# Kernel optimization log

Measured on AMD Instinct MI355X. Metric: run time of the kernel, lower is better.

The kernel has to match this reference:

```python
import jax, jax.numpy as jnp
import numpy as np

B, L, D_MODEL, N_HEADS = 2, 2048, 2048, 16
HEAD_DIM = D_MODEL // N_HEADS
EPS = 1e-6
ROPE_THETA = 10000.0


def rms_norm(x, scale):
    # normalize over head_dim, learnable per-dim scale (QKNorm)
    var = jnp.mean(jnp.square(x), axis=-1, keepdims=True)
    return x * jax.lax.rsqrt(var + EPS) * scale


def rope(x, offset=0):
    # x: [B, H, T, D]; rotate-half rotary embedding over flattened positions
    T, D = x.shape[-2], x.shape[-1]
    half = D // 2
    inv_freq = 1.0 / (ROPE_THETA ** (jnp.arange(0, half, dtype=jnp.float32) / half))
    pos = jnp.arange(T, dtype=jnp.float32) + offset
    ang = pos[:, None] * inv_freq[None, :]            # [T, half]
    cos, sin = jnp.cos(ang), jnp.sin(ang)
    x1, x2 = x[..., :half], x[..., half:]
    return jnp.concatenate([x1 * cos - x2 * sin, x1 * sin + x2 * cos], axis=-1)


def setup_inputs() -> dict:
    key = jax.random.key(0)
    ks = jax.random.split(key, 7)
    s = 1.0 / np.sqrt(D_MODEL)
    x = jax.random.normal(ks[0], (B, L, D_MODEL), dtype=jnp.float32)
    w_qkv = jax.random.uniform(ks[1], (D_MODEL, 3 * D_MODEL), jnp.float32, -s, s)
    b_qkv = jax.random.uniform(ks[2], (3 * D_MODEL,), jnp.float32, -s, s)
    q_scale = jnp.ones((HEAD_DIM,), jnp.float32)
    k_scale = jnp.ones((HEAD_DIM,), jnp.float32)
    w_out = jax.random.uniform(ks[3], (D_MODEL, D_MODEL), jnp.float32, -s, s)
    b_out = jax.random.uniform(ks[4], (D_MODEL,), jnp.float32, -s, s)
    mask = jnp.tril(jnp.ones((L, L), dtype=bool))   # causal block mask pattern
    return {"x": x, "w_qkv": w_qkv, "b_qkv": b_qkv, "q_scale": q_scale,
            "k_scale": k_scale, "w_out": w_out, "b_out": b_out, "mask": mask}


def reference(x, w_qkv, b_qkv, q_scale, k_scale, w_out, b_out, mask):
    b, t, _ = x.shape
    qkv = x @ w_qkv + b_qkv                                   # [B, T, 3*D]
    qkv = qkv.reshape(b, t, 3, N_HEADS, HEAD_DIM)
    q, k, v = jnp.moveaxis(qkv, 2, 0)                          # each [B, T, H, D]
    q = jnp.transpose(q, (0, 2, 1, 3))                         # [B, H, T, D]
    k = jnp.transpose(k, (0, 2, 1, 3))
    v = jnp.transpose(v, (0, 2, 1, 3))
    q = rms_norm(q, q_scale)
    k = rms_norm(k, k_scale)
    q = rope(q, offset=0)
    k = rope(k, offset=0)
    scores = jnp.einsum('bhqd,bhkd->bhqk', q, k) / np.sqrt(HEAD_DIM)
    scores = jnp.where(mask[None, None, :, :], scores, jnp.float32(-1e30))
    attn = jax.nn.softmax(scores, axis=-1)
    out = jnp.einsum('bhqk,bhkd->bhqd', attn, v)               # [B, H, T, D]
    out = jnp.transpose(out, (0, 2, 1, 3)).reshape(b, t, D_MODEL)
    return out @ w_out + b_out
```

## Files before the change

kernel.cpp:

```cpp
#include <hip/hip_runtime.h>
#include <hip/hip_bf16.h>
#include <stdint.h>


typedef unsigned short ushort8 __attribute__((ext_vector_type(8)));
typedef unsigned short ushort4v __attribute__((ext_vector_type(4)));
typedef short          bf16x8 __attribute__((ext_vector_type(8)));
typedef float          f32x4  __attribute__((ext_vector_type(4)));

#define B_   2
#define L_   2048
#define DM   2048
#define NH   16
#define HD   128
#define QKW  4096

__device__ __forceinline__ uint16_t f2bf(float f){
  uint32_t u = __builtin_bit_cast(uint32_t, f);
  u += 0x7FFFu + ((u >> 16) & 1u);
  return (uint16_t)(u >> 16);
}
__device__ __forceinline__ float bf2f(uint16_t h){
  uint32_t u = ((uint32_t)h) << 16;
  return __builtin_bit_cast(float, u);
}

#define GLD16(gp, lp) __builtin_amdgcn_global_load_lds( \
  (const __attribute__((address_space(1))) void*)(gp),  \
  (__attribute__((address_space(3))) void*)(lp), 16, 0, 0)

__global__ __launch_bounds__(256) void prep(
    const float* __restrict__ Wqkv, uint16_t* __restrict__ WqkvT,
    const float* __restrict__ Wout, uint16_t* __restrict__ WoutT,
    const float* __restrict__ x, uint16_t* __restrict__ xb,
    float* __restrict__ ct, float* __restrict__ st)
{
  __shared__ float T[64][65];
  const int bid = blockIdx.x;
  const int tid = threadIdx.x;

  if (bid < 4096){
    const float* W; uint16_t* Wt; int R = 2048, C; int rb, cb;
    if (bid < 3072){ W = Wqkv; Wt = WqkvT; C = 6144; rb = bid & 31; cb = bid >> 5; }
    else           { int i = bid - 3072; W = Wout; Wt = WoutT; C = 2048; rb = i & 31; cb = i >> 5; }
#pragma unroll
    for (int i=0;i<4;i++){
      int rr = i*16 + (tid >> 4);
      int cc = (tid & 15) * 4;
      float4 v = *(const float4*)(W + (size_t)(rb*64 + rr) * C + cb*64 + cc);
      T[rr][cc] = v.x; T[rr][cc+1] = v.y; T[rr][cc+2] = v.z; T[rr][cc+3] = v.w;
    }
    __syncthreads();
    const int oc = tid >> 2, rc = (tid & 3) * 16;
    ushort8 o0, o1;
#pragma unroll
    for (int j=0;j<8;j++){ o0[j] = f2bf(T[rc+j][oc]); o1[j] = f2bf(T[rc+8+j][oc]); }
    size_t ob = (size_t)(cb*64 + oc) * R + rb*64 + rc;
    *(ushort8*)(Wt + ob)     = o0;
    *(ushort8*)(Wt + ob + 8) = o1;
  } else if (bid < 8192){
    int i = (bid - 4096) * 256 + tid;
    const float4* xv = (const float4*)x;
    float4 a = xv[(size_t)i*2], b = xv[(size_t)i*2+1];
    ushort8 v;
    v[0]=f2bf(a.x); v[1]=f2bf(a.y); v[2]=f2bf(a.z); v[3]=f2bf(a.w);
    v[4]=f2bf(b.x); v[5]=f2bf(b.y); v[6]=f2bf(b.z); v[7]=f2bf(b.w);
    *(ushort8*)(xb + (size_t)i*8) = v;
  } else {
    int i = (bid - 8192) * 256 + tid;
    int t = i >> 6, d = i & 63;
    float invf = powf(10000.f, -(float)d * (1.f/64.f));
    float s, c;
    sincosf((float)t * invf, &s, &c);
    ct[i] = c; st[i] = s;
  }
}

template<int MODE>
__global__ __launch_bounds__(512, 2) void gemm8p(
    const uint16_t* __restrict__ A, const uint16_t* __restrict__ Bt,
    const float* __restrict__ bias, void* __restrict__ Cv, void* __restrict__ Cv2,
    int M, int N, int K, int nbn, int ldc,
    const float* __restrict__ qs, const float* __restrict__ ks,
    const float* __restrict__ ct, const float* __restrict__ st)
{
  __shared__ uint16_t LA[3*16384];
  __shared__ uint16_t LB[3*8192];
  __shared__ float sums[4][2][64];
  const int nwg = (M >> 8) * nbn;
  const int q8  = nwg >> 3;
  const int id  = ((int)blockIdx.x & 7) * q8 + ((int)blockIdx.x >> 3);
  const int bm = id / nbn, bn = id % nbn;
  const int tid = threadIdx.x;
  const int lane = tid & 63, w = tid >> 6;
  const int wm = w & 3, wn = w >> 2;
  const int l15 = lane & 15, lh = lane >> 4;
  const int NT = K >> 6;

  const int qs3 = ((lane & 7) ^ ((lane >> 3) & 7)) * 8;
  const uint16_t* gA_ = A  + (size_t)((bm << 8) + (w << 5) + (lane >> 3)) * K + qs3;
  const uint16_t* gB_ = Bt + (size_t)((bn << 7) + (w << 4) + (lane >> 3)) * K + qs3;
  uint16_t* lA_ = LA + (w << 11);
  uint16_t* lB_ = LB + (w << 10);

  const int sw0 = ((lh       ^ (l15 & 7)) << 3);
  const int sw1 = (((4 | lh) ^ (l15 & 7)) << 3);
  const int aoff = (((wm << 6) + l15) << 6);
  const int boff = (((wn << 5) + l15) << 6);
  const int bno[4] = {0, 1024, 4096, 5120};

  f32x4 acc[4][4];
#pragma unroll
  for (int i=0;i<4;i++)
#pragma unroll
    for (int j=0;j<4;j++) acc[i][j] = f32x4{0.f,0.f,0.f,0.f};

  auto STAGE_A = [&](int tt, int s, int i){
    GLD16(gA_ + (size_t)tt*64 + (size_t)(i*8)*K, lA_ + s*16384 + i*512);
  };
  auto STAGE_B = [&](int tt, int s, int i){
    GLD16(gB_ + (size_t)tt*64 + (size_t)(i*8)*K, lB_ + s*8192 + i*512);
  };

#pragma unroll
  for (int i=0;i<4;i++) STAGE_A(0, 0, i);
#pragma unroll
  for (int i=0;i<2;i++) STAGE_B(0, 0, i);
#pragma unroll
  for (int i=0;i<4;i++) STAGE_A(1, 1, i);
#pragma unroll
  for (int i=0;i<2;i++) STAGE_B(1, 1, i);
  asm volatile("s_waitcnt vmcnt(6)" ::: "memory");
  __builtin_amdgcn_s_barrier();

  int sl = 0, sl2 = 2;
  for (int t = 0; t < NT; ++t){
    const bool pf = (t + 2 < NT);
    const uint16_t* la = LA + sl*16384;
    const uint16_t* lb = LB + sl*8192;

    bf16x8 af0[4], bf0[4], af1[4], bf1[4];
#pragma unroll
    for (int mi=0;mi<4;mi++) af0[mi] = *(const bf16x8*)(la + aoff + mi*1024 + sw0);
#pragma unroll
    for (int ni=0;ni<4;ni++) bf0[ni] = *(const bf16x8*)(lb + boff + bno[ni] + sw0);
#pragma unroll
    for (int mi=0;mi<4;mi++) af1[mi] = *(const bf16x8*)(la + aoff + mi*1024 + sw1);
#pragma unroll
    for (int ni=0;ni<4;ni++) bf1[ni] = *(const bf16x8*)(lb + boff + bno[ni] + sw1);
    if (pf){
      STAGE_A(t+2, sl2, 0); STAGE_A(t+2, sl2, 1);
      STAGE_A(t+2, sl2, 2); STAGE_A(t+2, sl2, 3);
      STAGE_B(t+2, sl2, 0); STAGE_B(t+2, sl2, 1);
    }
    __builtin_amdgcn_s_setprio(1);
#pragma unroll
    for (int mi=0;mi<4;mi++)
#pragma unroll
      for (int ni=0;ni<4;ni++)
        acc[mi][ni] = __builtin_amdgcn_mfma_f32_16x16x32_bf16(af0[mi], bf0[ni], acc[mi][ni], 0, 0, 0);
#pragma unroll
    for (int mi=0;mi<4;mi++)
#pragma unroll
      for (int ni=0;ni<4;ni++)
        acc[mi][ni] = __builtin_amdgcn_mfma_f32_16x16x32_bf16(af1[mi], bf1[ni], acc[mi][ni], 0, 0, 0);
    __builtin_amdgcn_s_setprio(0);

    if (t < NT-2)       { asm volatile("s_waitcnt vmcnt(6)" ::: "memory"); }
    else if (t == NT-2) { asm volatile("s_waitcnt vmcnt(0)" ::: "memory"); }
    if (t < NT-1) __builtin_amdgcn_s_barrier();
    sl  = (sl  == 2) ? 0 : sl  + 1;
    sl2 = (sl2 == 2) ? 0 : sl2 + 1;
  }

  const int cm = (bm << 8) + (wm << 6);
  const int cn = (bn << 7);
  int dc[4];
#pragma unroll
  for (int ni=0;ni<4;ni++) dc[ni] = (wn<<5) + ((ni>>1)<<6) + ((ni&1)<<4) + l15;
  float bs[4];
#pragma unroll
  for (int ni=0;ni<4;ni++) bs[ni] = bias[cn + dc[ni]];

  if (MODE == 0){
#pragma unroll
    for (int mi=0;mi<4;mi++)
#pragma unroll
      for (int r=0;r<4;r++){
        int rowg = cm + mi*16 + lh*4 + r;
#pragma unroll
        for (int ni=0;ni<4;ni++)
          ((float*)Cv)[(size_t)rowg * ldc + cn + dc[ni]] = acc[mi][ni][r] + bs[ni];
      }
  } else {
    const int part = bn >> 4;
    if (part == 2){
      uint16_t* vtp = (uint16_t*)Cv2;
      const int h  = bn & 15;
      const int bb = cm >> 11;
      const int t0 = (cm & (L_-1)) + lh*4;
#pragma unroll
      for (int mi=0;mi<4;mi++){
#pragma unroll
        for (int ni=0;ni<4;ni++){
          ushort4v pk;
#pragma unroll
          for (int r=0;r<4;r++) pk[r] = f2bf(acc[mi][ni][r] + bs[ni]);
          *(ushort4v*)(vtp + ((size_t)((bb*16 + h)*128 + dc[ni]))*L_ + t0 + mi*16) = pk;
        }
      }
    } else {
      uint16_t* Cb = (uint16_t*)Cv;
      const float* scp = part ? ks : qs;
      float scv[4];
#pragma unroll
      for (int ni=0;ni<4;ni++) scv[ni] = scp[dc[ni]];
      float ssum[4][4];
#pragma unroll
      for (int mi=0;mi<4;mi++)
#pragma unroll
        for (int r=0;r<4;r++){
          float s = 0.f;
#pragma unroll
          for (int ni=0;ni<4;ni++){
            float v = acc[mi][ni][r] + bs[ni];
            acc[mi][ni][r] = v;
            s += v*v;
          }
          s += __shfl_xor(s, 1); s += __shfl_xor(s, 2);
          s += __shfl_xor(s, 4); s += __shfl_xor(s, 8);
          ssum[mi][r] = s;
        }
      if (l15 == 0){
#pragma unroll
        for (int mi=0;mi<4;mi++)
#pragma unroll
          for (int r=0;r<4;r++) sums[wm][wn][mi*16 + lh*4 + r] = ssum[mi][r];
      }
      __syncthreads();
      const int dd0 = (wn<<5) + l15, dd1 = dd0 + 16;
#pragma unroll
      for (int mi=0;mi<4;mi++){
#pragma unroll
        for (int r=0;r<4;r++){
          int rid = mi*16 + lh*4 + r;
          float tot = ssum[mi][r] + sums[wm][wn^1][rid];
          float iv = rsqrtf(tot * 0.0078125f + 1e-6f);
          int rowg = cm + rid;
          int t = rowg & (L_-1);
          float y0 = acc[mi][0][r] * iv * scv[0];
          float y1 = acc[mi][1][r] * iv * scv[1];
          float y2 = acc[mi][2][r] * iv * scv[2];
          float y3 = acc[mi][3][r] * iv * scv[3];
          float c0 = ct[t*64 + dd0], s0 = st[t*64 + dd0];
          float c1 = ct[t*64 + dd1], s1 = st[t*64 + dd1];
          size_t rb_ = (size_t)rowg * ldc + cn;
          Cb[rb_ + dc[0]] = f2bf(y0*c0 - y2*s0);
          Cb[rb_ + dc[1]] = f2bf(y1*c1 - y3*s1);
          Cb[rb_ + dc[2]] = f2bf(y0*s0 + y2*c0);
          Cb[rb_ + dc[3]] = f2bf(y1*s1 + y3*c1);
        }
      }
    }
  }
}

__global__ __launch_bounds__(256) void flash_attn(
    const uint16_t* __restrict__ qk, const uint16_t* __restrict__ vt,
    uint16_t* __restrict__ ao)
{
  const int qp = blockIdx.x;
  const int bh = blockIdx.y;
  const int b = bh >> 4, h = bh & 15;
  const int tid = threadIdx.x;
  const int lane = tid & 63, w = tid >> 6;
  const int l15 = lane & 15, lh = lane >> 4;

  __shared__ uint16_t Ks[64][136];
  __shared__ uint16_t Vs[128][72];
  __shared__ uint16_t Ps[4][16][72];

  const float SCL = 0.12751744f;

  for (int sel = 0; sel < 2; sel++){
    const int qb = sel ? (31 - qp) : qp;

    const size_t qrow = (size_t)b * L_ + qb*64 + w*16 + l15;
    const uint16_t* qp_ = qk + qrow * QKW + h * HD;
    bf16x8 qf[4];
#pragma unroll
    for (int c = 0; c < 4; c++) qf[c] = *(const bf16x8*)(qp_ + c*32 + lh*8);

    float m_s = -3.0e38f, l_s = 0.f;
    f32x4 oacc[8];
#pragma unroll
    for (int nt = 0; nt < 8; nt++) oacc[nt] = f32x4{0.f,0.f,0.f,0.f};

    const int ntile = qb + 1;
    ushort8 rk[4], rv[4];

#pragma unroll
    for (int i = 0; i < 4; i++){
      int g = i*256 + tid, row = g >> 4, c = g & 15;
      rk[i] = *(const ushort8*)(qk + ((size_t)b*L_ + row)*QKW + DM + h*HD + c*8);
    }
#pragma unroll
    for (int i = 0; i < 4; i++){
      int g = i*256 + tid, d = g >> 3, c = g & 7;
      rv[i] = *(const ushort8*)(vt + ((size_t)bh*HD + d)*L_ + c*8);
    }

    for (int kt = 0; kt < ntile; kt++){
      __syncthreads();
#pragma unroll
      for (int i = 0; i < 4; i++){ int g = i*256+tid; *(ushort8*)(&Ks[g>>4][(g&15)*8]) = rk[i]; }
#pragma unroll
      for (int i = 0; i < 4; i++){ int g = i*256+tid; *(ushort8*)(&Vs[g>>3][(g&7)*8]) = rv[i]; }
      __syncthreads();

      if (kt + 1 < ntile){
        const int k2 = (kt + 1) * 64;
#pragma unroll
        for (int i = 0; i < 4; i++){
          int g = i*256 + tid, row = g >> 4, c = g & 15;
          rk[i] = *(const ushort8*)(qk + ((size_t)b*L_ + k2 + row)*QKW + DM + h*HD + c*8);
        }
#pragma unroll
        for (int i = 0; i < 4; i++){
          int g = i*256 + tid, d = g >> 3, c = g & 7;
          rv[i] = *(const ushort8*)(vt + ((size_t)bh*HD + d)*L_ + k2 + c*8);
        }
      }

      f32x4 s[4];
#pragma unroll
      for (int nt = 0; nt < 4; nt++) s[nt] = f32x4{0.f,0.f,0.f,0.f};
      __builtin_amdgcn_s_setprio(1);
#pragma unroll
      for (int c = 0; c < 4; c++){
#pragma unroll
        for (int nt = 0; nt < 4; nt++){
          bf16x8 kf = *(const bf16x8*)(&Ks[nt*16 + l15][c*32 + lh*8]);
          s[nt] = __builtin_amdgcn_mfma_f32_16x16x32_bf16(kf, qf[c], s[nt], 0, 0, 0);
        }
      }
      __builtin_amdgcn_s_setprio(0);

      const bool diag = (kt == qb);
      const int qg = w*16 + l15;
      const int kb = lh*4;
#pragma unroll
      for (int nt = 0; nt < 4; nt++){
#pragma unroll
        for (int r = 0; r < 4; r++){
          float v = s[nt][r] * SCL;
          if (diag && (nt*16 + kb + r > qg)) v = -1.0e30f;
          s[nt][r] = v;
        }
      }
      float pm = s[0][0];
#pragma unroll
      for (int nt = 0; nt < 4; nt++)
#pragma unroll
        for (int r = 0; r < 4; r++) pm = fmaxf(pm, s[nt][r]);
      pm = fmaxf(pm, __shfl_xor(pm, 16));
      pm = fmaxf(pm, __shfl_xor(pm, 32));
      if (!__all(pm - m_s <= 8.0f)){
        float mn = fmaxf(m_s, pm);
        float alpha = exp2f(m_s - mn);
        m_s = mn; l_s *= alpha;
        float ar[4];
#pragma unroll
        for (int r = 0; r < 4; r++) ar[r] = __shfl(alpha, lh*4 + r);
#pragma unroll
        for (int nt = 0; nt < 8; nt++)
#pragma unroll
          for (int r = 0; r < 4; r++) oacc[nt][r] *= ar[r];
      }
      float rs = 0.f;
#pragma unroll
      for (int nt = 0; nt < 4; nt++){
        float p0 = exp2f(s[nt][0] - m_s);
        float p1 = exp2f(s[nt][1] - m_s);
        float p2 = exp2f(s[nt][2] - m_s);
        float p3 = exp2f(s[nt][3] - m_s);
        rs += (p0 + p1) + (p2 + p3);
        uint2 pk;
        pk.x = (uint32_t)f2bf(p0) | ((uint32_t)f2bf(p1) << 16);
        pk.y = (uint32_t)f2bf(p2) | ((uint32_t)f2bf(p3) << 16);
        *(uint2*)(&Ps[w][l15][nt*16 + kb]) = pk;
      }
      rs += __shfl_xor(rs, 16);
      rs += __shfl_xor(rs, 32);
      l_s += rs;

      asm volatile("s_waitcnt lgkmcnt(0)" ::: "memory");
      __builtin_amdgcn_s_setprio(1);
#pragma unroll
      for (int kc = 0; kc < 2; kc++){
        bf16x8 pf = *(const bf16x8*)(&Ps[w][l15][kc*32 + lh*8]);
#pragma unroll
        for (int nt = 0; nt < 8; nt++){
          bf16x8 vf = *(const bf16x8*)(&Vs[nt*16 + l15][kc*32 + lh*8]);
          oacc[nt] = __builtin_amdgcn_mfma_f32_16x16x32_bf16(pf, vf, oacc[nt], 0, 0, 0);
        }
      }
      __builtin_amdgcn_s_setprio(0);
    }
    float invl[4];
#pragma unroll
    for (int r = 0; r < 4; r++) invl[r] = 1.f / __shfl(l_s, lh*4 + r);
#pragma unroll
    for (int nt = 0; nt < 8; nt++){
#pragma unroll
      for (int r = 0; r < 4; r++){
        float v = oacc[nt][r] * invl[r];
        size_t row = (size_t)b*L_ + qb*64 + w*16 + lh*4 + r;
        ao[row * DM + h*HD + nt*16 + l15] = f2bf(v);
      }
    }
  }
}

extern "C" void kernel_launch(void* const* d_in, const int* in_sizes, int n_in,
                              void* d_out, int out_size, void* d_ws, size_t ws_size,
                              hipStream_t stream)
{
  (void)in_sizes; (void)n_in; (void)out_size; (void)ws_size;
  const float* x       = (const float*)d_in[0];
  const float* w_qkv   = (const float*)d_in[1];
  const float* b_qkv   = (const float*)d_in[2];
  const float* q_scale = (const float*)d_in[3];
  const float* k_scale = (const float*)d_in[4];
  const float* w_out   = (const float*)d_in[5];
  const float* b_out   = (const float*)d_in[6];
  float* out = (float*)d_out;

  char* ws = (char*)d_ws;
  uint16_t* qk    = (uint16_t*)(ws);
  uint16_t* vt    = (uint16_t*)(ws + 33554432);
  uint16_t* reg1  = (uint16_t*)(ws + 50331648);
  uint16_t* wqkvT = (uint16_t*)(ws + 67108864);
  uint16_t* woutT = (uint16_t*)(ws + 92274688);
  float*    ct    = (float*)(ws + 100663296);
  float*    st    = ct + 131072;

  uint16_t* xb = reg1;
  uint16_t* ao = reg1;

  prep        <<<8704, 256, 0, stream>>>(w_qkv, wqkvT, w_out, woutT, x, xb, ct, st);
  gemm8p<1>   <<<768, 512, 0, stream>>>(xb, wqkvT, b_qkv, qk, vt,
                                        4096, 6144, 2048, 48, 4096,
                                        q_scale, k_scale, ct, st);
  flash_attn  <<<dim3(16, 32), 256, 0, stream>>>(qk, vt, ao);
  gemm8p<0>   <<<256, 512, 0, stream>>>(ao, woutT, b_out, out, nullptr,
                                        4096, 2048, 2048, 16, 2048,
                                        nullptr, nullptr, nullptr, nullptr);
}
```

Baseline: 259.9 us.

## Double-buffer K/V tiles in LDS with one barrier per iteration

Turns the K and V shared-memory tiles into two buffers. The next tile is written into the alternate buffer at the start of each iteration, while the global prefetch now runs two tiles ahead. This cuts the two barriers per key tile down to one and lets LDS stores overlap with compute on the current tile. In exchange, LDS use roughly doubles (about 71KB total), which may lower how many blocks fit per CU, and the register prefetch now reaches further ahead.

```diff
diff --git a/kernel.cpp b/kernel.cpp
--- a/kernel.cpp
+++ b/kernel.cpp
@@ -276,8 +276,8 @@
   const int lane = tid & 63, w = tid >> 6;
   const int l15 = lane & 15, lh = lane >> 4;
 
-  __shared__ uint16_t Ks[64][136];
-  __shared__ uint16_t Vs[128][72];
+  __shared__ uint16_t Ks[2][64][136];
+  __shared__ uint16_t Vs[2][128][72];
   __shared__ uint16_t Ps[4][16][72];
 
   const float SCL = 0.12751744f;
@@ -299,6 +299,7 @@
     const int ntile = qb + 1;
     ushort8 rk[4], rv[4];
 
+    __syncthreads();
 #pragma unroll
     for (int i = 0; i < 4; i++){
       int g = i*256 + tid, row = g >> 4, c = g & 15;
@@ -309,26 +310,44 @@
       int g = i*256 + tid, d = g >> 3, c = g & 7;
       rv[i] = *(const ushort8*)(vt + ((size_t)bh*HD + d)*L_ + c*8);
     }
+#pragma unroll
+    for (int i = 0; i < 4; i++){ int g = i*256+tid; *(ushort8*)(&Ks[0][g>>4][(g&15)*8]) = rk[i]; }
+#pragma unroll
+    for (int i = 0; i < 4; i++){ int g = i*256+tid; *(ushort8*)(&Vs[0][g>>3][(g&7)*8]) = rv[i]; }
+    if (ntile > 1){
+#pragma unroll
+      for (int i = 0; i < 4; i++){
+        int g = i*256 + tid, row = g >> 4, c = g & 15;
+        rk[i] = *(const ushort8*)(qk + ((size_t)b*L_ + 64 + row)*QKW + DM + h*HD + c*8);
+      }
+#pragma unroll
+      for (int i = 0; i < 4; i++){
+        int g = i*256 + tid, d = g >> 3, c = g & 7;
+        rv[i] = *(const ushort8*)(vt + ((size_t)bh*HD + d)*L_ + 64 + c*8);
+      }
+    }
+    __syncthreads();
 
     for (int kt = 0; kt < ntile; kt++){
-      __syncthreads();
-#pragma unroll
-      for (int i = 0; i < 4; i++){ int g = i*256+tid; *(ushort8*)(&Ks[g>>4][(g&15)*8]) = rk[i]; }
-#pragma unroll
-      for (int i = 0; i < 4; i++){ int g = i*256+tid; *(ushort8*)(&Vs[g>>3][(g&7)*8]) = rv[i]; }
-      __syncthreads();
+      const int c = kt & 1;
 
       if (kt + 1 < ntile){
-        const int k2 = (kt + 1) * 64;
+#pragma unroll
+        for (int i = 0; i < 4; i++){ int g = i*256+tid; *(ushort8*)(&Ks[c^1][g>>4][(g&15)*8]) = rk[i]; }
+#pragma unroll
+        for (int i = 0; i < 4; i++){ int g = i*256+tid; *(ushort8*)(&Vs[c^1][g>>3][(g&7)*8]) = rv[i]; }
+      }
+      if (kt + 2 < ntile){
+        const int k2 = (kt + 2) * 64;
 #pragma unroll
         for (int i = 0; i < 4; i++){
-          int g = i*256 + tid, row = g >> 4, c = g & 15;
-          rk[i] = *(const ushort8*)(qk + ((size_t)b*L_ + k2 + row)*QKW + DM + h*HD + c*8);
+          int g = i*256 + tid, row = g >> 4, cc = g & 15;
+          rk[i] = *(const ushort8*)(qk + ((size_t)b*L_ + k2 + row)*QKW + DM + h*HD + cc*8);
         }
 #pragma unroll
         for (int i = 0; i < 4; i++){
-          int g = i*256 + tid, d = g >> 3, c = g & 7;
-          rv[i] = *(const ushort8*)(vt + ((size_t)bh*HD + d)*L_ + k2 + c*8);
+          int g = i*256 + tid, d = g >> 3, cc = g & 7;
+          rv[i] = *(const ushort8*)(vt + ((size_t)bh*HD + d)*L_ + k2 + cc*8);
         }
       }
 
@@ -337,11 +356,11 @@
       for (int nt = 0; nt < 4; nt++) s[nt] = f32x4{0.f,0.f,0.f,0.f};
       __builtin_amdgcn_s_setprio(1);
 #pragma unroll
-      for (int c = 0; c < 4; c++){
+      for (int cc = 0; cc < 4; cc++){
 #pragma unroll
         for (int nt = 0; nt < 4; nt++){
-          bf16x8 kf = *(const bf16x8*)(&Ks[nt*16 + l15][c*32 + lh*8]);
-          s[nt] = __builtin_amdgcn_mfma_f32_16x16x32_bf16(kf, qf[c], s[nt], 0, 0, 0);
+          bf16x8 kf = *(const bf16x8*)(&Ks[c][nt*16 + l15][cc*32 + lh*8]);
+          s[nt] = __builtin_amdgcn_mfma_f32_16x16x32_bf16(kf, qf[cc], s[nt], 0, 0, 0);
         }
       }
       __builtin_amdgcn_s_setprio(0);
@@ -401,11 +420,13 @@
         bf16x8 pf = *(const bf16x8*)(&Ps[w][l15][kc*32 + lh*8]);
 #pragma unroll
         for (int nt = 0; nt < 8; nt++){
-          bf16x8 vf = *(const bf16x8*)(&Vs[nt*16 + l15][kc*32 + lh*8]);
+          bf16x8 vf = *(const bf16x8*)(&Vs[c][nt*16 + l15][kc*32 + lh*8]);
           oacc[nt] = __builtin_amdgcn_mfma_f32_16x16x32_bf16(pf, vf, oacc[nt], 0, 0, 0);
         }
       }
       __builtin_amdgcn_s_setprio(0);
+
+      if (kt + 1 < ntile) __syncthreads();
     }
     float invl[4];
 #pragma unroll
```

Measured after the change: 261.9 us. No clear change (+0.8%).
